# Kernel tuning notes

Measured on AMD Instinct MI355X. Metric: run time of the kernel, lower is better.

Reference implementation:

```python
import jax, jax.numpy as jnp
import numpy as np

DIST_MULT = 0.1
CLIP_LOW = 0.0
EPS = 1e-6


def setup_inputs() -> dict:
    key = jax.random.key(0)
    k1, _ = jax.random.split(key)
    x_msg_binned = jax.random.normal(k1, (8, 64, 512, 16), dtype=jnp.float32)
    msk = jnp.ones((8, 64, 512, 1), dtype=jnp.float32)
    return {"x_msg_binned": x_msg_binned, "msk": msk}


def reference(x_msg_binned, msk):
    # A: (B, bins, N, F) masked node features
    A = x_msg_binned * msk
    na = jnp.sum(A * A, axis=-1)  # (B, bins, N)
    # Gram matrix: (B, bins, N, N)
    G = jnp.einsum("bknf,bkmf->bknm", A, A)
    D = jnp.sqrt(jnp.maximum(na[..., :, None] - 2.0 * G + na[..., None, :], EPS))
    dm = jnp.exp(-DIST_MULT * D)[..., None]  # (B, bins, N, N, 1)
    return jnp.clip(dm, CLIP_LOW, 1.0)
```

## Files before the change

kernel.cpp:

```cpp
#include <hip/hip_runtime.h>


typedef float f32x4 __attribute__((ext_vector_type(4)));

#define NEG_DIST_LOG2E (-0.14426950408889634f)
#define EPS_F 1e-6f

__global__ __launch_bounds__(256) void node_pair_gaussian_kernel(
    const float* __restrict__ x,
    const float* __restrict__ msk,
    float* __restrict__ out)
{
    __shared__ __align__(16) float lds_n[16][128];
    __shared__ __align__(16) float lds_m[16][128];
    __shared__ __align__(16) float na_n[128];
    __shared__ __align__(16) float na_m[128];

    const int tid   = threadIdx.x;
    const int tile  = blockIdx.x;
    const int slice = blockIdx.y;
    const int n0 = (tile >> 2) << 7;
    const int m0 = (tile & 3) << 7;

    const float* xs = x   + (size_t)slice * (512 * 16);
    const float* ms = msk + (size_t)slice * 512;

    #pragma unroll
    for (int it = 0; it < 2; ++it) {
        const int task = tid + it * 256;
        const int node = task & 127;
        const int f4   = task >> 7;
        {
            const f32x4 v = *(const f32x4*)(xs + (size_t)(n0 + node) * 16 + f4 * 4);
            const float mm = ms[n0 + node];
            lds_n[f4 * 4 + 0][node] = v.x * mm;
            lds_n[f4 * 4 + 1][node] = v.y * mm;
            lds_n[f4 * 4 + 2][node] = v.z * mm;
            lds_n[f4 * 4 + 3][node] = v.w * mm;
        }
        {
            const f32x4 v = *(const f32x4*)(xs + (size_t)(m0 + node) * 16 + f4 * 4);
            const float mm = ms[m0 + node];
            lds_m[f4 * 4 + 0][node] = v.x * mm;
            lds_m[f4 * 4 + 1][node] = v.y * mm;
            lds_m[f4 * 4 + 2][node] = v.z * mm;
            lds_m[f4 * 4 + 3][node] = v.w * mm;
        }
    }
    __syncthreads();

    {
        const int node = tid & 127;
        float s = 0.0f;
        if (tid < 128) {
            #pragma unroll
            for (int f = 0; f < 16; ++f) s = fmaf(lds_m[f][node], lds_m[f][node], s);
            na_m[node] = s;
        } else {
            #pragma unroll
            for (int f = 0; f < 16; ++f) s = fmaf(lds_n[f][node], lds_n[f][node], s);
            na_n[node] = s;
        }
    }
    __syncthreads();

    const int tx = tid & 15;
    const int ty = tid >> 4;

    float acc[8][8];
    #pragma unroll
    for (int i = 0; i < 8; ++i)
        #pragma unroll
        for (int j = 0; j < 8; ++j) acc[i][j] = 0.0f;

    #pragma unroll
    for (int f = 0; f < 16; ++f) {
        const f32x4 a0 = *(const f32x4*)&lds_n[f][ty * 4];
        const f32x4 a1 = *(const f32x4*)&lds_n[f][64 + ty * 4];
        const f32x4 b0 = *(const f32x4*)&lds_m[f][tx * 4];
        const f32x4 b1 = *(const f32x4*)&lds_m[f][64 + tx * 4];
        const float an[8] = {a0.x, a0.y, a0.z, a0.w, a1.x, a1.y, a1.z, a1.w};
        const float am[8] = {b0.x, b0.y, b0.z, b0.w, b1.x, b1.y, b1.z, b1.w};
        #pragma unroll
        for (int i = 0; i < 8; ++i)
            #pragma unroll
            for (int j = 0; j < 8; ++j)
                acc[i][j] = fmaf(an[i], am[j], acc[i][j]);
    }

    const f32x4 nn0 = *(const f32x4*)&na_n[ty * 4];
    const f32x4 nn1 = *(const f32x4*)&na_n[64 + ty * 4];
    const f32x4 nm0 = *(const f32x4*)&na_m[tx * 4];
    const f32x4 nm1 = *(const f32x4*)&na_m[64 + tx * 4];
    const float nn[8] = {nn0.x, nn0.y, nn0.z, nn0.w, nn1.x, nn1.y, nn1.z, nn1.w};
    const float nm[8] = {nm0.x, nm0.y, nm0.z, nm0.w, nm1.x, nm1.y, nm1.z, nm1.w};

    float* outs = out + (size_t)slice * (512 * 512) + (size_t)n0 * 512 + m0;

    #pragma unroll
    for (int i = 0; i < 8; ++i) {
        const int row = (i < 4) ? (ty * 4 + i) : (64 + ty * 4 + (i - 4));
        float r[8];
        #pragma unroll
        for (int j = 0; j < 8; ++j) {
            float s = nn[i] + nm[j] - 2.0f * acc[i][j];
            s = fmaxf(s, EPS_F);
            const float d = __builtin_amdgcn_sqrtf(s);
            const float e = __builtin_amdgcn_exp2f(d * NEG_DIST_LOG2E);
            r[j] = fminf(e, 1.0f);
        }
        f32x4 w0 = {r[0], r[1], r[2], r[3]};
        f32x4 w1 = {r[4], r[5], r[6], r[7]};
        __builtin_nontemporal_store(w0, (f32x4*)(outs + (size_t)row * 512 + tx * 4));
        __builtin_nontemporal_store(w1, (f32x4*)(outs + (size_t)row * 512 + 64 + tx * 4));
    }
}

extern "C" void kernel_launch(void* const* d_in, const int* in_sizes, int n_in,
                              void* d_out, int out_size, void* d_ws, size_t ws_size,
                              hipStream_t stream) {
    const float* x   = (const float*)d_in[0];
    const float* msk = (const float*)d_in[1];
    float* out = (float*)d_out;

    dim3 grid(16, 512);
    node_pair_gaussian_kernel<<<grid, 256, 0, stream>>>(x, msk, out);
}
```

Measured before the change: 530.2 us.

## Compute Gram tile with fp16 MFMA instead of fp32 FMA outer product

Stores masked features in LDS as fp16 in node-major layout and computes each 128x128 Gram tile with 16x16x16 f16 MFMA instructions, with each wave covering a 32-column slice. It aims to cut the scalar FMA work and register pressure of the 8x8 per-thread outer product. In exchange, inputs lose precision to fp16, and the output store pattern changes to 64-byte row segments per lane group, which may coalesce less well.

```diff
diff --git a/kernel.cpp b/kernel.cpp
--- a/kernel.cpp
+++ b/kernel.cpp
@@ -1,7 +1,8 @@
 #include <hip/hip_runtime.h>
 
 
-typedef float f32x4 __attribute__((ext_vector_type(4)));
+typedef float    f32x4 __attribute__((ext_vector_type(4)));
+typedef _Float16 f16x4 __attribute__((ext_vector_type(4)));
 
 #define NEG_DIST_LOG2E (-0.14426950408889634f)
 #define EPS_F 1e-6f
@@ -11,8 +12,8 @@
     const float* __restrict__ msk,
     float* __restrict__ out)
 {
-    __shared__ __align__(16) float lds_n[16][128];
-    __shared__ __align__(16) float lds_m[16][128];
+    __shared__ __align__(16) _Float16 lds_n[128][20];
+    __shared__ __align__(16) _Float16 lds_m[128][20];
     __shared__ __align__(16) float na_n[128];
     __shared__ __align__(16) float na_m[128];
 
@@ -33,86 +34,83 @@
         {
             const f32x4 v = *(const f32x4*)(xs + (size_t)(n0 + node) * 16 + f4 * 4);
             const float mm = ms[n0 + node];
-            lds_n[f4 * 4 + 0][node] = v.x * mm;
-            lds_n[f4 * 4 + 1][node] = v.y * mm;
-            lds_n[f4 * 4 + 2][node] = v.z * mm;
-            lds_n[f4 * 4 + 3][node] = v.w * mm;
+            f16x4 h = { (_Float16)(v.x * mm), (_Float16)(v.y * mm),
+                        (_Float16)(v.z * mm), (_Float16)(v.w * mm) };
+            *(f16x4*)&lds_n[node][f4 * 4] = h;
         }
         {
             const f32x4 v = *(const f32x4*)(xs + (size_t)(m0 + node) * 16 + f4 * 4);
             const float mm = ms[m0 + node];
-            lds_m[f4 * 4 + 0][node] = v.x * mm;
-            lds_m[f4 * 4 + 1][node] = v.y * mm;
-            lds_m[f4 * 4 + 2][node] = v.z * mm;
-            lds_m[f4 * 4 + 3][node] = v.w * mm;
+            f16x4 h = { (_Float16)(v.x * mm), (_Float16)(v.y * mm),
+                        (_Float16)(v.z * mm), (_Float16)(v.w * mm) };
+            *(f16x4*)&lds_m[node][f4 * 4] = h;
         }
     }
     __syncthreads();
 
     {
         const int node = tid & 127;
+        const _Float16* p = (tid < 128) ? &lds_m[node][0] : &lds_n[node][0];
         float s = 0.0f;
-        if (tid < 128) {
-            #pragma unroll
-            for (int f = 0; f < 16; ++f) s = fmaf(lds_m[f][node], lds_m[f][node], s);
-            na_m[node] = s;
-        } else {
-            #pragma unroll
-            for (int f = 0; f < 16; ++f) s = fmaf(lds_n[f][node], lds_n[f][node], s);
-            na_n[node] = s;
+        #pragma unroll
+        for (int f4 = 0; f4 < 4; ++f4) {
+            const f16x4 h = *(const f16x4*)&p[f4 * 4];
+            const float a0 = (float)h.x, a1 = (float)h.y;
+            const float a2 = (float)h.z, a3 = (float)h.w;
+            s = fmaf(a0, a0, s); s = fmaf(a1, a1, s);
+            s = fmaf(a2, a2, s); s = fmaf(a3, a3, s);
         }
+        if (tid < 128) na_m[node] = s; else na_n[node] = s;
     }
     __syncthreads();
 
-    const int tx = tid & 15;
-    const int ty = tid >> 4;
+    const int lane = tid & 63;
+    const int wv   = tid >> 6;
+    const int lr   = lane & 15;
+    const int q    = lane >> 4;
+    const int mb   = wv * 32;
 
-    float acc[8][8];
+    f16x4 afr[2];
     #pragma unroll
-    for (int i = 0; i < 8; ++i)
+    for (int a = 0; a < 2; ++a)
+        afr[a] = *(const f16x4*)&lds_m[mb + a * 16 + lr][q * 4];
+    f16x4 bfr[8];
+    #pragma unroll
+    for (int b = 0; b < 8; ++b)
+        bfr[b] = *(const f16x4*)&lds_n[b * 16 + lr][q * 4];
+
+    f32x4 acc[8][2];
+    #pragma unroll
+    for (int b = 0; b < 8; ++b)
         #pragma unroll
-        for (int j = 0; j < 8; ++j) acc[i][j] = 0.0f;
+        for (int a = 0; a < 2; ++a) {
+            f32x4 z = {0.0f, 0.0f, 0.0f, 0.0f};
+            acc[b][a] = __builtin_amdgcn_mfma_f32_16x16x16f16(afr[a], bfr[b], z, 0, 0, 0);
+        }
+
+    f32x4 nm[2];
+    nm[0] = *(const f32x4*)&na_m[mb + q * 4];
+    nm[1] = *(const f32x4*)&na_m[mb + 16 + q * 4];
+
+    float* outs = out + (size_t)slice * (512 * 512) + (size_t)n0 * 512 + (m0 + mb);
 
     #pragma unroll
-    for (int f = 0; f < 16; ++f) {
-        const f32x4 a0 = *(const f32x4*)&lds_n[f][ty * 4];
-        const f32x4 a1 = *(const f32x4*)&lds_n[f][64 + ty * 4];
-        const f32x4 b0 = *(const f32x4*)&lds_m[f][tx * 4];
-        const f32x4 b1 = *(const f32x4*)&lds_m[f][64 + tx * 4];
-        const float an[8] = {a0.x, a0.y, a0.z, a0.w, a1.x, a1.y, a1.z, a1.w};
-        const float am[8] = {b0.x, b0.y, b0.z, b0.w, b1.x, b1.y, b1.z, b1.w};
+    for (int b = 0; b < 8; ++b) {
+        const float nn = na_n[b * 16 + lr];
+        const size_t rowoff = (size_t)(b * 16 + lr) * 512;
         #pragma unroll
-        for (int i = 0; i < 8; ++i)
+        for (int a = 0; a < 2; ++a) {
+            f32x4 r;
             #pragma unroll
-            for (int j = 0; j < 8; ++j)
-                acc[i][j] = fmaf(an[i], am[j], acc[i][j]);
-    }
-
-    const f32x4 nn0 = *(const f32x4*)&na_n[ty * 4];
-    const f32x4 nn1 = *(const f32x4*)&na_n[64 + ty * 4];
-    const f32x4 nm0 = *(const f32x4*)&na_m[tx * 4];
-    const f32x4 nm1 = *(const f32x4*)&na_m[64 + tx * 4];
-    const float nn[8] = {nn0.x, nn0.y, nn0.z, nn0.w, nn1.x, nn1.y, nn1.z, nn1.w};
-    const float nm[8] = {nm0.x, nm0.y, nm0.z, nm0.w, nm1.x, nm1.y, nm1.z, nm1.w};
-
-    float* outs = out + (size_t)slice * (512 * 512) + (size_t)n0 * 512 + m0;
-
-    #pragma unroll
-    for (int i = 0; i < 8; ++i) {
-        const int row = (i < 4) ? (ty * 4 + i) : (64 + ty * 4 + (i - 4));
-        float r[8];
-        #pragma unroll
-        for (int j = 0; j < 8; ++j) {
-            float s = nn[i] + nm[j] - 2.0f * acc[i][j];
-            s = fmaxf(s, EPS_F);
-            const float d = __builtin_amdgcn_sqrtf(s);
-            const float e = __builtin_amdgcn_exp2f(d * NEG_DIST_LOG2E);
-            r[j] = fminf(e, 1.0f);
+            for (int j = 0; j < 4; ++j) {
+                float s = fmaf(-2.0f, acc[b][a][j], nn + nm[a][j]);
+                s = fmaxf(s, EPS_F);
+                const float d = __builtin_amdgcn_sqrtf(s);
+                const float e = __builtin_amdgcn_exp2f(d * NEG_DIST_LOG2E);
+                r[j] = fminf(e, 1.0f);
+            }
+            __builtin_nontemporal_store(r, (f32x4*)(outs + rowoff + a * 16 + q * 4));
         }
-        f32x4 w0 = {r[0], r[1], r[2], r[3]};
-        f32x4 w1 = {r[4], r[5], r[6], r[7]};
-        __builtin_nontemporal_store(w0, (f32x4*)(outs + (size_t)row * 512 + tx * 4));
-        __builtin_nontemporal_store(w1, (f32x4*)(outs + (size_t)row * 512 + 64 + tx * 4));
     }
 }
 
```

Measured after the change: 601.4 us. +13.4%, slower.

## Tile full output rows per block and fuse row-norm computation into loads

Applied to the files above, without the earlier changes.

Each 512-thread block now computes a 64x512 strip of one slice instead of a 128x128 tile, so every wave writes full contiguous 2KB output rows. Squared norms are computed during the global load with lane shuffles, removing a separate LDS pass and one barrier. LDS arrays are padded. The cost is reloading the whole slice's features per strip and higher LDS use per block, which may lower occupancy.

```diff
diff --git a/kernel.cpp b/kernel.cpp
--- a/kernel.cpp
+++ b/kernel.cpp
@@ -5,67 +5,60 @@
 
 #define NEG_DIST_LOG2E (-0.14426950408889634f)
 #define EPS_F 1e-6f
+#define LDM 516
+#define LDN 68
 
-__global__ __launch_bounds__(256) void node_pair_gaussian_kernel(
+__global__ __launch_bounds__(512) void node_pair_gaussian_kernel(
     const float* __restrict__ x,
     const float* __restrict__ msk,
     float* __restrict__ out)
 {
-    __shared__ __align__(16) float lds_n[16][128];
-    __shared__ __align__(16) float lds_m[16][128];
-    __shared__ __align__(16) float na_n[128];
-    __shared__ __align__(16) float na_m[128];
+    __shared__ __align__(16) float lds_m[16][LDM];
+    __shared__ __align__(16) float lds_n[16][LDN];
+    __shared__ __align__(16) float na_m[512];
+    __shared__ __align__(16) float na_n[64];
 
     const int tid   = threadIdx.x;
-    const int tile  = blockIdx.x;
-    const int slice = blockIdx.y;
-    const int n0 = (tile >> 2) << 7;
-    const int m0 = (tile & 3) << 7;
+    const int slice = blockIdx.x;
+    const int r0    = blockIdx.y << 6;
 
     const float* xs = x   + (size_t)slice * (512 * 16);
     const float* ms = msk + (size_t)slice * 512;
 
     #pragma unroll
-    for (int it = 0; it < 2; ++it) {
-        const int task = tid + it * 256;
-        const int node = task & 127;
-        const int f4   = task >> 7;
-        {
-            const f32x4 v = *(const f32x4*)(xs + (size_t)(n0 + node) * 16 + f4 * 4);
-            const float mm = ms[n0 + node];
-            lds_n[f4 * 4 + 0][node] = v.x * mm;
-            lds_n[f4 * 4 + 1][node] = v.y * mm;
-            lds_n[f4 * 4 + 2][node] = v.z * mm;
-            lds_n[f4 * 4 + 3][node] = v.w * mm;
-        }
-        {
-            const f32x4 v = *(const f32x4*)(xs + (size_t)(m0 + node) * 16 + f4 * 4);
-            const float mm = ms[m0 + node];
-            lds_m[f4 * 4 + 0][node] = v.x * mm;
-            lds_m[f4 * 4 + 1][node] = v.y * mm;
-            lds_m[f4 * 4 + 2][node] = v.z * mm;
-            lds_m[f4 * 4 + 3][node] = v.w * mm;
-        }
+    for (int it = 0; it < 4; ++it) {
+        const int c    = tid + it * 512;
+        const int node = c >> 2;
+        const int f4   = (c & 3) * 4;
+        const f32x4 v  = *(const f32x4*)(xs + (size_t)c * 4);
+        const float mm = ms[node];
+        lds_m[f4 + 0][node] = v.x * mm;
+        lds_m[f4 + 1][node] = v.y * mm;
+        lds_m[f4 + 2][node] = v.z * mm;
+        lds_m[f4 + 3][node] = v.w * mm;
+        float p = (v.x * v.x + v.y * v.y + v.z * v.z + v.w * v.w) * (mm * mm);
+        p += __shfl_xor(p, 1);
+        p += __shfl_xor(p, 2);
+        if ((tid & 3) == 0) na_m[node] = p;
+    }
+    if (tid < 256) {
+        const int node = tid >> 2;
+        const int f4   = (tid & 3) * 4;
+        const f32x4 v  = *(const f32x4*)(xs + (size_t)(r0 + node) * 16 + f4);
+        const float mm = ms[r0 + node];
+        lds_n[f4 + 0][node] = v.x * mm;
+        lds_n[f4 + 1][node] = v.y * mm;
+        lds_n[f4 + 2][node] = v.z * mm;
+        lds_n[f4 + 3][node] = v.w * mm;
+        float p = (v.x * v.x + v.y * v.y + v.z * v.z + v.w * v.w) * (mm * mm);
+        p += __shfl_xor(p, 1);
+        p += __shfl_xor(p, 2);
+        if ((tid & 3) == 0) na_n[node] = p;
     }
     __syncthreads();
 
-    {
-        const int node = tid & 127;
-        float s = 0.0f;
-        if (tid < 128) {
-            #pragma unroll
-            for (int f = 0; f < 16; ++f) s = fmaf(lds_m[f][node], lds_m[f][node], s);
-            na_m[node] = s;
-        } else {
-            #pragma unroll
-            for (int f = 0; f < 16; ++f) s = fmaf(lds_n[f][node], lds_n[f][node], s);
-            na_n[node] = s;
-        }
-    }
-    __syncthreads();
-
-    const int tx = tid & 15;
-    const int ty = tid >> 4;
+    const int lane = tid & 63;
+    const int w8   = (tid >> 6) << 3;
 
     float acc[8][8];
     #pragma unroll
@@ -75,10 +68,10 @@
 
     #pragma unroll
     for (int f = 0; f < 16; ++f) {
-        const f32x4 a0 = *(const f32x4*)&lds_n[f][ty * 4];
-        const f32x4 a1 = *(const f32x4*)&lds_n[f][64 + ty * 4];
-        const f32x4 b0 = *(const f32x4*)&lds_m[f][tx * 4];
-        const f32x4 b1 = *(const f32x4*)&lds_m[f][64 + tx * 4];
+        const f32x4 a0 = *(const f32x4*)&lds_n[f][w8];
+        const f32x4 a1 = *(const f32x4*)&lds_n[f][w8 + 4];
+        const f32x4 b0 = *(const f32x4*)&lds_m[f][lane * 4];
+        const f32x4 b1 = *(const f32x4*)&lds_m[f][256 + lane * 4];
         const float an[8] = {a0.x, a0.y, a0.z, a0.w, a1.x, a1.y, a1.z, a1.w};
         const float am[8] = {b0.x, b0.y, b0.z, b0.w, b1.x, b1.y, b1.z, b1.w};
         #pragma unroll
@@ -88,22 +81,21 @@
                 acc[i][j] = fmaf(an[i], am[j], acc[i][j]);
     }
 
-    const f32x4 nn0 = *(const f32x4*)&na_n[ty * 4];
-    const f32x4 nn1 = *(const f32x4*)&na_n[64 + ty * 4];
-    const f32x4 nm0 = *(const f32x4*)&na_m[tx * 4];
-    const f32x4 nm1 = *(const f32x4*)&na_m[64 + tx * 4];
+    const f32x4 nn0 = *(const f32x4*)&na_n[w8];
+    const f32x4 nn1 = *(const f32x4*)&na_n[w8 + 4];
+    const f32x4 nm0 = *(const f32x4*)&na_m[lane * 4];
+    const f32x4 nm1 = *(const f32x4*)&na_m[256 + lane * 4];
     const float nn[8] = {nn0.x, nn0.y, nn0.z, nn0.w, nn1.x, nn1.y, nn1.z, nn1.w};
     const float nm[8] = {nm0.x, nm0.y, nm0.z, nm0.w, nm1.x, nm1.y, nm1.z, nm1.w};
 
-    float* outs = out + (size_t)slice * (512 * 512) + (size_t)n0 * 512 + m0;
+    float* outs = out + (size_t)slice * (512 * 512) + (size_t)r0 * 512;
 
     #pragma unroll
     for (int i = 0; i < 8; ++i) {
-        const int row = (i < 4) ? (ty * 4 + i) : (64 + ty * 4 + (i - 4));
         float r[8];
         #pragma unroll
         for (int j = 0; j < 8; ++j) {
-            float s = nn[i] + nm[j] - 2.0f * acc[i][j];
+            float s = fmaf(-2.0f, acc[i][j], nn[i] + nm[j]);
             s = fmaxf(s, EPS_F);
             const float d = __builtin_amdgcn_sqrtf(s);
             const float e = __builtin_amdgcn_exp2f(d * NEG_DIST_LOG2E);
@@ -111,8 +103,9 @@
         }
         f32x4 w0 = {r[0], r[1], r[2], r[3]};
         f32x4 w1 = {r[4], r[5], r[6], r[7]};
-        __builtin_nontemporal_store(w0, (f32x4*)(outs + (size_t)row * 512 + tx * 4));
-        __builtin_nontemporal_store(w1, (f32x4*)(outs + (size_t)row * 512 + 64 + tx * 4));
+        float* rowp = outs + (size_t)(w8 + i) * 512;
+        __builtin_nontemporal_store(w0, (f32x4*)(rowp + lane * 4));
+        __builtin_nontemporal_store(w1, (f32x4*)(rowp + 256 + lane * 4));
     }
 }
 
@@ -123,6 +116,6 @@
     const float* msk = (const float*)d_in[1];
     float* out = (float*)d_out;
 
-    dim3 grid(16, 512);
-    node_pair_gaussian_kernel<<<grid, 256, 0, stream>>>(x, msk, out);
+    dim3 grid(512, 8);
+    node_pair_gaussian_kernel<<<grid, 512, 0, stream>>>(x, msk, out);
 }
```

New measurement: 525.5 us. About the same (-0.9%).
